# Performance work log

Hardware: AMD Instinct MI355X
Metric: run time of the kernel (lower is better)

## Reference

```python
import jax, jax.numpy as jnp
import numpy as np

OBS_LEN, BATCH, IN_DIM, HID = 20, 2048, 512, 1024


def setup_inputs() -> dict:
    key = jax.random.key(0)
    ks = jax.random.split(key, 9)
    s_ih = 1.0 / np.sqrt(HID)  # torch LSTMCell init scale (uniform); use normal*scale for simplicity
    return {
        "obs_traj": jax.random.normal(ks[0], (OBS_LEN, BATCH, 2), jnp.float32),
        "h0": jax.random.normal(ks[1], (BATCH, HID), jnp.float32),
        "c0": jax.random.normal(ks[2], (BATCH, HID), jnp.float32),
        "W_emb": jax.random.normal(ks[3], (IN_DIM, 2), jnp.float32) * 0.5,
        "b_emb": jax.random.normal(ks[4], (IN_DIM,), jnp.float32) * 0.5,
        "W_ih": jax.random.normal(ks[5], (4 * HID, IN_DIM), jnp.float32) * s_ih,
        "W_hh": jax.random.normal(ks[6], (4 * HID, HID), jnp.float32) * s_ih,
        "b_ih": jax.random.normal(ks[7], (4 * HID,), jnp.float32) * s_ih,
        "b_hh": jax.random.normal(ks[8], (4 * HID,), jnp.float32) * s_ih,
    }


def reference(obs_traj, h0, c0, W_emb, b_emb, W_ih, W_hh, b_ih, b_hh):
    # input embedding: Linear(2 -> IN_DIM) applied to all timesteps at once
    # [T, B, 2] @ [2, IN_DIM] -> [T, B, IN_DIM]
    x_emb = jnp.einsum('tbi,hi->tbh', obs_traj, W_emb) + b_emb
    x_emb = x_emb[:OBS_LEN]

    H = h0.shape[-1]
    bias = b_ih + b_hh  # fold both biases once

    def step(carry, x_t):
        h, c = carry
        # gates: [B, 4H], PyTorch gate order i, f, g, o
        gates = x_t @ W_ih.T + h @ W_hh.T + bias
        i_g = jax.nn.sigmoid(gates[:, 0 * H:1 * H])
        f_g = jax.nn.sigmoid(gates[:, 1 * H:2 * H])
        g_g = jnp.tanh(gates[:, 2 * H:3 * H])
        o_g = jax.nn.sigmoid(gates[:, 3 * H:4 * H])
        c_new = f_g * c + i_g * g_g
        h_new = o_g * jnp.tanh(c_new)
        return (h_new, c_new), None

    (h_final, _), _ = jax.lax.scan(step, (h0, c0), x_emb)
    return h_final
```

## Files before the change

kernel.cpp:

```cpp
#include <hip/hip_runtime.h>

#define B_SZ 2048
#define HID  1024
#define G4   4096
#define IN_D 512
#define T_LEN 20
#define NT   (HID/32)

#define POFF(r, q) ((r)*32 + ((((q) ^ (((r) >> 1) & 3))) << 3))

typedef __attribute__((ext_vector_type(8))) _Float16 f16x8;
typedef __attribute__((ext_vector_type(4))) float f32x4;
typedef const __attribute__((address_space(1))) void* gas_p;
typedef __attribute__((address_space(3))) void* las_p;

__device__ __forceinline__ float bf2f(ushort u){
  union { unsigned int i; float f; } v; v.i = ((unsigned int)u) << 16; return v.f;
}
__device__ __forceinline__ ushort f2bf(float f){
  union { float f; unsigned int i; } v; v.f = f;
  unsigned int r = v.i + 0x7fffu + ((v.i >> 16) & 1u);
  return (ushort)(r >> 16);
}
__device__ __forceinline__ ushort f2h(float f){
  _Float16 h = (_Float16)f;
  union { _Float16 h; ushort u; } v; v.h = h; return v.u;
}
__device__ __forceinline__ float rdv(const void* p, long idx, int fl){
  return fl ? ((const float*)p)[idx] : bf2f(((const ushort*)p)[idx]);
}
__device__ __forceinline__ float sigm(float x){ return 1.0f/(1.0f + __expf(-x)); }
__device__ __forceinline__ float tanh_f(float x){
  float e = __expf(2.0f*x);
  return 1.0f - 2.0f/(e + 1.0f);
}

__global__ void detect_dtype(const ushort* __restrict__ h0bits, int* __restrict__ flag){
  int weird = 0;
  for (int i = 0; i < 256; i += 2){
    float a = fabsf(bf2f(h0bits[i]));
    if (!(a >= 1e-8f && a <= 1e4f)) weird++;
  }
  *flag = (weird >= 32) ? 1 : 0;
}

__global__ void canon(const void* __restrict__ h0, const void* __restrict__ c0,
                      const void* __restrict__ whh, const int* __restrict__ flag,
                      ushort* __restrict__ hA,
                      float* __restrict__ c_state,
                      ushort* __restrict__ wpk){
  const int fl = *flag;
  long i = (long)blockIdx.x * 256 + threadIdx.x;
  const long N1 = (long)B_SZ * HID;
  const long N3 = (long)G4 * HID;
  if (i < N1){
    const int b = (int)(i >> 10), j = (int)(i & 1023);
    const int r = b & 127, q = (j >> 3) & 3;
    const long po = ((long)(b >> 7)*32 + (j >> 5))*4096 + POFF(r, q) + (j & 7);
    hA[po] = f2h(rdv(h0, i, fl));
    return;
  }
  i -= N1;
  if (i < N1){ c_state[i] = rdv(c0, i, fl); return; }
  i -= N1;
  if (i < N3){
    const int n = (int)(i >> 10), k = (int)(i & 1023);
    const int g = n >> 10, j = n & 1023;
    const int nb = j >> 5, r = g*32 + (j & 31);
    const int kt = k >> 5, q = (k >> 3) & 3;
    const long base = ((long)(nb*32 + kt))*4096 + POFF(r, q) + (k & 7);
    wpk[base] = f2h(rdv(whh, i, fl));
  }
}

__global__ void fold_emb(const void* __restrict__ Wih, const void* __restrict__ Wemb,
                         const void* __restrict__ bemb, const void* __restrict__ bih,
                         const void* __restrict__ bhh, const int* __restrict__ flag,
                         float* __restrict__ M0, float* __restrict__ M1, float* __restrict__ Beff){
  const int n = blockIdx.x;
  const int lane = threadIdx.x;
  const int fl = *flag;
  float s0 = 0.f, s1 = 0.f, sb = 0.f;
  for (int j = lane; j < IN_D; j += 64){
    float w  = rdv(Wih, (long)n*IN_D + j, fl);
    float e0 = rdv(Wemb, 2L*j, fl);
    float e1 = rdv(Wemb, 2L*j + 1, fl);
    float be = rdv(bemb, j, fl);
    s0 += w*e0; s1 += w*e1; sb += w*be;
  }
  #pragma unroll
  for (int off = 32; off > 0; off >>= 1){
    s0 += __shfl_down(s0, off, 64);
    s1 += __shfl_down(s1, off, 64);
    sb += __shfl_down(sb, off, 64);
  }
  if (lane == 0){
    M0[n] = s0; M1[n] = s1;
    Beff[n] = sb + rdv(bih, n, fl) + rdv(bhh, n, fl);
  }
}

__global__ __launch_bounds__(256, 2)
void lstm_step(const ushort* __restrict__ hin, ushort* __restrict__ hout,
               void* __restrict__ out_final,
               float* __restrict__ c_state,
               const ushort* __restrict__ wpk,
               const float* __restrict__ M0, const float* __restrict__ M1,
               const float* __restrict__ Beff,
               const void* __restrict__ obs_raw, int t_step,
               const int* __restrict__ flag, int is_final)
{
  __shared__ __align__(16) ushort lds[3*8192];

  const int tid  = threadIdx.x;
  const int wave = tid >> 6;
  const int lane = tid & 63;
  const int l15  = lane & 15;
  const int quad = lane >> 4;
  const int wm   = wave & 1;
  const int wn   = wave >> 1;

  const int bid = blockIdx.x;
  const int xcd = bid & 7, u = bid >> 3;
  const int mb  = ((xcd & 1) << 3) | (u & 7);
  const int nb  = ((xcd >> 1) << 3) | (u >> 3);
  const int n0  = nb << 5;

  f32x4 acc[4][4];
  #pragma unroll
  for (int g = 0; g < 4; g++)
    #pragma unroll
    for (int mt = 0; mt < 4; mt++)
      acc[g][mt] = (f32x4){0.f, 0.f, 0.f, 0.f};

  const ushort* aB = hin + (size_t)mb*32*4096;
  const ushort* wB = wpk + (size_t)nb*32*4096;

  const int dOff = tid*8;

  #define DMA_TILE(kt, buf) do {                                              \
    const ushort* s0 = aB + (size_t)(kt)*4096;                                \
    const ushort* s1 = wB + (size_t)(kt)*4096;                                \
    ushort* d = &lds[(buf)*8192];                                             \
    __builtin_amdgcn_global_load_lds((gas_p)(s0+dOff),      (las_p)(d+dOff),      16,0,0); \
    __builtin_amdgcn_global_load_lds((gas_p)(s0+2048+dOff), (las_p)(d+2048+dOff), 16,0,0); \
    __builtin_amdgcn_global_load_lds((gas_p)(s1+dOff),      (las_p)(d+4096+dOff), 16,0,0); \
    __builtin_amdgcn_global_load_lds((gas_p)(s1+2048+dOff), (las_p)(d+6144+dOff), 16,0,0); \
  } while (0)

  int offA[4], offB[4];
  #pragma unroll
  for (int mt = 0; mt < 4; mt++) {
    const int r = wm*64 + mt*16 + l15;
    offA[mt] = POFF(r, quad);
  }
  #pragma unroll
  for (int g = 0; g < 4; g++) {
    const int r = g*32 + wn*16 + l15;
    offB[g] = 4096 + POFF(r, quad);
  }

  DMA_TILE(0, 0);
  DMA_TILE(1, 1);
  asm volatile("s_waitcnt vmcnt(4)" ::: "memory");
  asm volatile("s_barrier" ::: "memory");

  int cur = 0;
  #pragma unroll 1
  for (int kt = 0; kt < NT; kt++) {
    const int sb = cur * 8192;

    f16x8 a[4], b[4];
    #pragma unroll
    for (int mt = 0; mt < 4; mt++)
      a[mt] = *reinterpret_cast<const f16x8*>(&lds[sb + offA[mt]]);
    #pragma unroll
    for (int g = 0; g < 4; g++)
      b[g] = *reinterpret_cast<const f16x8*>(&lds[sb + offB[g]]);

    if (kt + 2 < NT) {
      int stg = cur + 2; if (stg >= 3) stg -= 3;
      DMA_TILE(kt + 2, stg);
    }

    #pragma unroll
    for (int g = 0; g < 4; g++)
      #pragma unroll
      for (int mt = 0; mt < 4; mt++)
        acc[g][mt] = __builtin_amdgcn_mfma_f32_16x16x32_f16(a[mt], b[g], acc[g][mt], 0, 0, 0);

    if (kt + 2 < NT) asm volatile("s_waitcnt vmcnt(4)" ::: "memory");
    else             asm volatile("s_waitcnt vmcnt(0)" ::: "memory");
    asm volatile("s_barrier" ::: "memory");
    __builtin_amdgcn_sched_barrier(0);

    cur = (cur == 2) ? 0 : cur + 1;
  }
  #undef DMA_TILE

  const int fl = *flag;
  const int j = n0 + wn*16 + l15;
  float bi[4], m0v[4], m1v[4];
  #pragma unroll
  for (int g = 0; g < 4; g++) {
    bi[g]  = Beff[g*HID + j];
    m0v[g] = M0[g*HID + j];
    m1v[g] = M1[g*HID + j];
  }
  const int jq = (j >> 3) & 3;
  #pragma unroll
  for (int mt = 0; mt < 4; mt++) {
    #pragma unroll
    for (int r = 0; r < 4; r++) {
      const int bl7 = wm*64 + mt*16 + quad*4 + r;
      const int b   = mb*128 + bl7;
      const long oidx = ((long)t_step * B_SZ + b) * 2;
      const float o0 = rdv(obs_raw, oidx, fl);
      const float o1 = rdv(obs_raw, oidx + 1, fl);
      const size_t off = (size_t)b*HID + j;
      float pi = acc[0][mt][r] + o0*m0v[0] + o1*m1v[0] + bi[0];
      float pf = acc[1][mt][r] + o0*m0v[1] + o1*m1v[1] + bi[1];
      float pg = acc[2][mt][r] + o0*m0v[2] + o1*m1v[2] + bi[2];
      float po = acc[3][mt][r] + o0*m0v[3] + o1*m1v[3] + bi[3];
      float cn = sigm(pf)*c_state[off] + sigm(pi)*tanh_f(pg);
      float hn = sigm(po)*tanh_f(cn);
      c_state[off] = cn;
      if (is_final) {
        if (fl) ((float*)out_final)[off] = hn;
        else    ((ushort*)out_final)[off] = f2bf(hn);
      } else {
        const long hpo = ((long)mb*32 + (j >> 5))*4096 + POFF(bl7, jq) + (j & 7);
        hout[hpo] = f2h(hn);
      }
    }
  }
}

extern "C" void kernel_launch(void* const* d_in, const int* in_sizes, int n_in,
                              void* d_out, int out_size, void* d_ws, size_t ws_size,
                              hipStream_t stream) {
  const void* obs  = d_in[0];
  const void* h0   = d_in[1];
  const void* c0   = d_in[2];
  const void* Wemb = d_in[3];
  const void* bemb = d_in[4];
  const void* Wih  = d_in[5];
  const void* Whh  = d_in[6];
  const void* bih  = d_in[7];
  const void* bhh  = d_in[8];

  char* w = (char*)d_ws;
  int*    flag    = (int*)w;
  float*  M0      = (float*)(w + 256);
  float*  M1      = M0 + G4;
  float*  Beff    = M1 + G4;
  float*  c_state = Beff + G4;
  ushort* wpk     = (ushort*)(c_state + (size_t)B_SZ*HID);
  ushort* hA      = wpk + (size_t)G4*HID;
  ushort* hB      = hA + (size_t)B_SZ*HID;

  detect_dtype<<<1, 1, 0, stream>>>((const ushort*)h0, flag);

  long totalCanon = 2L*B_SZ*HID + (long)G4*HID;
  canon<<<(int)((totalCanon + 255)/256), 256, 0, stream>>>(
      h0, c0, Whh, flag, hA, c_state, wpk);

  fold_emb<<<G4, 64, 0, stream>>>(Wih, Wemb, bemb, bih, bhh, flag, M0, M1, Beff);

  for (int t = 0; t < T_LEN; t++) {
    const ushort* ih = (t & 1) ? hB : hA;
    ushort* oh = (t & 1) ? hA : hB;
    lstm_step<<<512, 256, 0, stream>>>(ih, oh, d_out, c_state,
                                       wpk, M0, M1, Beff,
                                       obs, t, flag, (t == T_LEN - 1) ? 1 : 0);
  }
}
```

Baseline: 673.3 us.

## Give each wave private double-buffered LDS tiles to drop block barriers

Each wave now loads its own copy of the A and W sub-tiles into a private double-buffered LDS region. Waves wait only on their own vmcnt and lgkmcnt, so the per-iteration s_barrier is gone. This is meant to remove block-wide synchronisation stalls in the K loop. The cost is redundant global loads, since A rows are shared by waves with the same wm and W by waves with the same wn, plus larger LDS use (64KB), which may reduce occupancy.

```diff
diff --git a/kernel.cpp b/kernel.cpp
--- a/kernel.cpp
+++ b/kernel.cpp
@@ -110,7 +110,7 @@
                const void* __restrict__ obs_raw, int t_step,
                const int* __restrict__ flag, int is_final)
 {
-  __shared__ __align__(16) ushort lds[3*8192];
+  __shared__ __align__(16) ushort lds[8*4096];
 
   const int tid  = threadIdx.x;
   const int wave = tid >> 6;
@@ -133,68 +133,64 @@
     for (int mt = 0; mt < 4; mt++)
       acc[g][mt] = (f32x4){0.f, 0.f, 0.f, 0.f};
 
-  const ushort* aB = hin + (size_t)mb*32*4096;
-  const ushort* wB = wpk + (size_t)nb*32*4096;
-
-  const int dOff = tid*8;
-
-  #define DMA_TILE(kt, buf) do {                                              \
-    const ushort* s0 = aB + (size_t)(kt)*4096;                                \
-    const ushort* s1 = wB + (size_t)(kt)*4096;                                \
-    ushort* d = &lds[(buf)*8192];                                             \
-    __builtin_amdgcn_global_load_lds((gas_p)(s0+dOff),      (las_p)(d+dOff),      16,0,0); \
-    __builtin_amdgcn_global_load_lds((gas_p)(s0+2048+dOff), (las_p)(d+2048+dOff), 16,0,0); \
-    __builtin_amdgcn_global_load_lds((gas_p)(s1+dOff),      (las_p)(d+4096+dOff), 16,0,0); \
-    __builtin_amdgcn_global_load_lds((gas_p)(s1+2048+dOff), (las_p)(d+6144+dOff), 16,0,0); \
+  const ushort* aB = hin + (size_t)mb*32*4096 + (size_t)wm*2048;
+  const ushort* wB = wpk + (size_t)nb*32*4096 + (size_t)wn*512;
+
+  ushort* wbase = &lds[wave * 8192];
+  const int lOff = lane * 8;
+
+  #define DMA_TILE(kt, bsel) do {                                             \
+    const ushort* sa = aB + (size_t)(kt)*4096;                                \
+    const ushort* sw = wB + (size_t)(kt)*4096;                                \
+    ushort* d = wbase + (bsel)*4096;                                          \
+    __builtin_amdgcn_global_load_lds((gas_p)(sa + 0*512  + lOff), (las_p)(d + 0*512  + lOff), 16,0,0); \
+    __builtin_amdgcn_global_load_lds((gas_p)(sa + 1*512  + lOff), (las_p)(d + 1*512  + lOff), 16,0,0); \
+    __builtin_amdgcn_global_load_lds((gas_p)(sa + 2*512  + lOff), (las_p)(d + 2*512  + lOff), 16,0,0); \
+    __builtin_amdgcn_global_load_lds((gas_p)(sa + 3*512  + lOff), (las_p)(d + 3*512  + lOff), 16,0,0); \
+    __builtin_amdgcn_global_load_lds((gas_p)(sw + 0*1024 + lOff), (las_p)(d + 2048 + 0*512 + lOff), 16,0,0); \
+    __builtin_amdgcn_global_load_lds((gas_p)(sw + 1*1024 + lOff), (las_p)(d + 2048 + 1*512 + lOff), 16,0,0); \
+    __builtin_amdgcn_global_load_lds((gas_p)(sw + 2*1024 + lOff), (las_p)(d + 2048 + 2*512 + lOff), 16,0,0); \
+    __builtin_amdgcn_global_load_lds((gas_p)(sw + 3*1024 + lOff), (las_p)(d + 2048 + 3*512 + lOff), 16,0,0); \
   } while (0)
 
   int offA[4], offB[4];
   #pragma unroll
   for (int mt = 0; mt < 4; mt++) {
-    const int r = wm*64 + mt*16 + l15;
-    offA[mt] = POFF(r, quad);
+    const int rp = mt*16 + l15;
+    offA[mt] = POFF(rp, quad);
   }
   #pragma unroll
   for (int g = 0; g < 4; g++) {
-    const int r = g*32 + wn*16 + l15;
-    offB[g] = 4096 + POFF(r, quad);
+    const int sw_ = ((wn*16 + l15) >> 1) & 3;
+    offB[g] = 2048 + g*512 + l15*32 + ((quad ^ sw_) << 3);
   }
 
   DMA_TILE(0, 0);
   DMA_TILE(1, 1);
-  asm volatile("s_waitcnt vmcnt(4)" ::: "memory");
-  asm volatile("s_barrier" ::: "memory");
-
-  int cur = 0;
+
   #pragma unroll 1
   for (int kt = 0; kt < NT; kt++) {
-    const int sb = cur * 8192;
-
+    if (kt + 1 < NT) asm volatile("s_waitcnt vmcnt(8)" ::: "memory");
+    else             asm volatile("s_waitcnt vmcnt(0)" ::: "memory");
+
+    const int sb = (kt & 1) * 4096;
     f16x8 a[4], b[4];
     #pragma unroll
     for (int mt = 0; mt < 4; mt++)
-      a[mt] = *reinterpret_cast<const f16x8*>(&lds[sb + offA[mt]]);
+      a[mt] = *reinterpret_cast<const f16x8*>(&wbase[sb + offA[mt]]);
     #pragma unroll
     for (int g = 0; g < 4; g++)
-      b[g] = *reinterpret_cast<const f16x8*>(&lds[sb + offB[g]]);
-
-    if (kt + 2 < NT) {
-      int stg = cur + 2; if (stg >= 3) stg -= 3;
-      DMA_TILE(kt + 2, stg);
-    }
+      b[g] = *reinterpret_cast<const f16x8*>(&wbase[sb + offB[g]]);
+
+    asm volatile("s_waitcnt lgkmcnt(0)" ::: "memory");
+    __builtin_amdgcn_sched_barrier(0);
+    if (kt + 2 < NT) DMA_TILE(kt + 2, kt & 1);
 
     #pragma unroll
     for (int g = 0; g < 4; g++)
       #pragma unroll
       for (int mt = 0; mt < 4; mt++)
         acc[g][mt] = __builtin_amdgcn_mfma_f32_16x16x32_f16(a[mt], b[g], acc[g][mt], 0, 0, 0);
-
-    if (kt + 2 < NT) asm volatile("s_waitcnt vmcnt(4)" ::: "memory");
-    else             asm volatile("s_waitcnt vmcnt(0)" ::: "memory");
-    asm volatile("s_barrier" ::: "memory");
-    __builtin_amdgcn_sched_barrier(0);
-
-    cur = (cur == 2) ? 0 : cur + 1;
   }
   #undef DMA_TILE
 
```

Result: slower. 772.6 us (+14.7%).
